# Kernel optimization log

Hardware: AMD Instinct MI355X
Metric: run time of the kernel (lower is better)

Reference implementation:

```python
import jax, jax.numpy as jnp
import numpy as np

C = 128  # n_filters; input channels must equal n_filters due to residual


def setup_inputs() -> dict:
    key = jax.random.key(0)
    kx, kw = jax.random.split(key)
    x = jax.random.normal(kx, (8, 64, 512, C), dtype=jnp.float32)
    # 1x1 conv, no bias == dense over channel axis: [C, 2C]
    W_qkv = jax.random.normal(kw, (C, 2 * C), dtype=jnp.float32) * (1.0 / np.sqrt(C))
    return {"x": x, "W_qkv": W_qkv}


def reference(x, W_qkv):
    # qkv: [B,H,W,2C]; split -> qk [B,H,W,C] -> q,k [B,H,W,C/2]; v [B,H,W,C]
    qkv = jnp.einsum('bhwc,cd->bhwd', x, W_qkv)
    half = C // 2
    q = qkv[..., :half]
    k = qkv[..., half:C]
    v = qkv[..., C:]
    # scores over the W (time) axis; NOTE: original applies no 1/sqrt(d) scaling
    scores = jnp.einsum('bhqc,bhkc->bhqk', q, k)  # [B,H,W,W]
    w = jax.nn.softmax(scores, axis=-1)
    y = jnp.einsum('bhqk,bhkc->bhqc', w, v)  # [B,H,W,C]
    y = x + y  # with_skip_connection=True
    return (y, w)
```

## Files before the change

kernel.cpp:

```cpp
#include <hip/hip_runtime.h>
#include <hip/hip_bf16.h>

typedef short s16x8 __attribute__((ext_vector_type(8)));
typedef float f32x4 __attribute__((ext_vector_type(4)));

#define MFMA_BF16(a,b,c) __builtin_amdgcn_mfma_f32_16x16x32_bf16((a),(b),(c),0,0,0)

static __device__ __forceinline__ unsigned short f2bf(float f){
  unsigned u = __builtin_bit_cast(unsigned, f);
  u += 0x7fffu + ((u >> 16) & 1u);
  return (unsigned short)(u >> 16);
}
static __device__ __forceinline__ float bf2f(unsigned short h){
  unsigned u = ((unsigned)h) << 16;
  return __builtin_bit_cast(float, u);
}
static __device__ __forceinline__ int swzi(int row, int col, int lw){
  const int chunk = (col >> 3) ^ ((row ^ (row >> 3)) & 7);
  return row*lw + (chunk << 3) + (col & 7);
}

__global__ __launch_bounds__(128) void k0_wt(const float* __restrict__ W,
                                             unsigned short* __restrict__ wtH,
                                             unsigned short* __restrict__ wtL){
  const int n = blockIdx.x;
  const int c = threadIdx.x;
  const float v = W[(size_t)c*256 + n];
  const unsigned short h = f2bf(v);
  wtH[n*128 + c] = h;
  wtL[n*128 + c] = f2bf(v - bf2f(h));
}

__global__ __launch_bounds__(512,2) void k1_qkv(const float* __restrict__ x,
    const unsigned short* __restrict__ wtH, const unsigned short* __restrict__ wtL,
    unsigned short* __restrict__ qh, unsigned short* __restrict__ ql,
    unsigned short* __restrict__ kh, unsigned short* __restrict__ kl,
    unsigned short* __restrict__ vT){
  __shared__ unsigned short xh[16384], xl[16384];
  const int t = threadIdx.x;
  const int lane = t & 63, wid = t >> 6;
  const int li = lane & 15, g = lane >> 4;
  const int m0 = blockIdx.x * 128;
  const int wm = wid >> 2, wn = wid & 3;

  {
    const int row = t >> 2, cb = (t & 3) * 32;
    const float* src = x + (size_t)(m0 + row)*128 + cb;
    #pragma unroll
    for (int gg = 0; gg < 4; ++gg){
      const float4 v0 = ((const float4*)src)[2*gg];
      const float4 v1 = ((const float4*)src)[2*gg + 1];
      const float vv[8] = {v0.x,v0.y,v0.z,v0.w,v1.x,v1.y,v1.z,v1.w};
      s16x8 h, l;
      #pragma unroll
      for (int j = 0; j < 8; ++j){
        const unsigned short hb = f2bf(vv[j]);
        h[j] = (short)hb;
        l[j] = (short)f2bf(vv[j] - bf2f(hb));
      }
      const int idx = swzi(row, cb + 8*gg, 128);
      *(s16x8*)&xh[idx] = h;
      *(s16x8*)&xl[idx] = l;
    }
  }
  __syncthreads();

  {
    f32x4 acc[4][2] = {};
    #pragma unroll
    for (int ks = 0; ks < 4; ++ks){
      const int col = ks*32 + g*8;
      s16x8 ah[4], al[4];
      #pragma unroll
      for (int mi = 0; mi < 4; ++mi){
        const int idx = swzi(wm*64 + mi*16 + li, col, 128);
        ah[mi] = *(const s16x8*)&xh[idx];
        al[mi] = *(const s16x8*)&xl[idx];
      }
      #pragma unroll
      for (int ni = 0; ni < 2; ++ni){
        const size_t boff = (size_t)(wn*32 + ni*16 + li)*128 + col;
        const s16x8 bh = *(const s16x8*)(wtH + boff);
        const s16x8 bl = *(const s16x8*)(wtL + boff);
        #pragma unroll
        for (int mi = 0; mi < 4; ++mi){
          acc[mi][ni] = MFMA_BF16(bh, ah[mi], acc[mi][ni]);
          acc[mi][ni] = MFMA_BF16(bh, al[mi], acc[mi][ni]);
          acc[mi][ni] = MFMA_BF16(bl, ah[mi], acc[mi][ni]);
        }
      }
    }
    #pragma unroll
    for (int mi = 0; mi < 4; ++mi)
      #pragma unroll
      for (int ni = 0; ni < 2; ++ni){
        const int pos = m0 + wm*64 + mi*16 + li;
        const int och = wn*32 + ni*16 + g*4;
        ushort4 hv, lv;
        #pragma unroll
        for (int r = 0; r < 4; ++r){
          const float v = acc[mi][ni][r];
          const unsigned short hb = f2bf(v);
          ((unsigned short*)&hv)[r] = hb;
          ((unsigned short*)&lv)[r] = f2bf(v - bf2f(hb));
        }
        const size_t off = (size_t)pos*64 + (och & 63);
        if (wn < 2){ *(ushort4*)&qh[off] = hv; *(ushort4*)&ql[off] = lv; }
        else       { *(ushort4*)&kh[off] = hv; *(ushort4*)&kl[off] = lv; }
      }
  }

  {
    f32x4 acc[4][2] = {};
    #pragma unroll
    for (int ks = 0; ks < 4; ++ks){
      const int col = ks*32 + g*8;
      s16x8 ah[4], al[4];
      #pragma unroll
      for (int mi = 0; mi < 4; ++mi){
        const int idx = swzi(wm*64 + mi*16 + li, col, 128);
        ah[mi] = *(const s16x8*)&xh[idx];
        al[mi] = *(const s16x8*)&xl[idx];
      }
      #pragma unroll
      for (int ni = 0; ni < 2; ++ni){
        const size_t boff = (size_t)(128 + wn*32 + ni*16 + li)*128 + col;
        const s16x8 bh = *(const s16x8*)(wtH + boff);
        const s16x8 bl = *(const s16x8*)(wtL + boff);
        #pragma unroll
        for (int mi = 0; mi < 4; ++mi){
          acc[mi][ni] = MFMA_BF16(ah[mi], bh, acc[mi][ni]);
          acc[mi][ni] = MFMA_BF16(ah[mi], bl, acc[mi][ni]);
          acc[mi][ni] = MFMA_BF16(al[mi], bh, acc[mi][ni]);
        }
      }
    }
    #pragma unroll
    for (int mi = 0; mi < 4; ++mi)
      #pragma unroll
      for (int ni = 0; ni < 2; ++ni){
        const int growb = m0 + wm*64 + mi*16 + g*4;
        const int ch = wn*32 + ni*16 + li;
        const int head = growb >> 9, posb = growb & 511;
        ushort4 pv;
        #pragma unroll
        for (int r = 0; r < 4; ++r)
          ((unsigned short*)&pv)[r] = f2bf(acc[mi][ni][r]);
        *(ushort4*)&vT[((size_t)head << 16) + ch*512 + posb] = pv;
      }
  }
}

__global__ __launch_bounds__(256,4) void k2_attn(
    const unsigned short* __restrict__ qh, const unsigned short* __restrict__ ql,
    const unsigned short* __restrict__ kh, const unsigned short* __restrict__ kl,
    const unsigned short* __restrict__ vT, const float* __restrict__ x,
    float* __restrict__ y, float* __restrict__ wout){
  __shared__ unsigned short wlds[16384];
  __shared__ float redm[128], reds[128];

  const int t = threadIdx.x;
  const int lane = t & 63, wid = t >> 6;
  const int li = lane & 15, g = lane >> 4;
  const int bi = blockIdx.x;
  const int head = (bi & 7) + 8 * (bi >> 7);
  const int qt = (bi >> 3) & 15;
  const size_t hbase = (size_t)head * 512;
  const int q0 = qt * 32;
  const int kbase = wid * 128;

  f32x4 acc[2][8] = {};
  #pragma unroll
  for (int ks = 0; ks < 2; ++ks){
    const int col = ks*32 + g*8;
    s16x8 qbh[2], qbl[2];
    #pragma unroll
    for (int qj = 0; qj < 2; ++qj){
      const size_t aoff = (hbase + q0 + qj*16 + li)*64 + col;
      qbh[qj] = *(const s16x8*)(qh + aoff);
      qbl[qj] = *(const s16x8*)(ql + aoff);
    }
    #pragma unroll
    for (int ni = 0; ni < 8; ++ni){
      const size_t boff = (hbase + kbase + ni*16 + li)*64 + col;
      const s16x8 ah = *(const s16x8*)(kh + boff);
      const s16x8 al = *(const s16x8*)(kl + boff);
      #pragma unroll
      for (int qj = 0; qj < 2; ++qj){
        acc[qj][ni] = MFMA_BF16(ah, qbh[qj], acc[qj][ni]);
        acc[qj][ni] = MFMA_BF16(al, qbh[qj], acc[qj][ni]);
        acc[qj][ni] = MFMA_BF16(ah, qbl[qj], acc[qj][ni]);
      }
    }
  }

  float fsc[2];
  #pragma unroll
  for (int qj = 0; qj < 2; ++qj){
    float m = acc[qj][0][0];
    #pragma unroll
    for (int ni = 0; ni < 8; ++ni)
      #pragma unroll
      for (int r = 0; r < 4; ++r) m = fmaxf(m, acc[qj][ni][r]);
    m = fmaxf(m, __shfl_xor(m, 16));
    m = fmaxf(m, __shfl_xor(m, 32));
    float s = 0.f;
    #pragma unroll
    for (int ni = 0; ni < 8; ++ni)
      #pragma unroll
      for (int r = 0; r < 4; ++r){
        const float e = __expf(acc[qj][ni][r] - m);
        acc[qj][ni][r] = e;
        s += e;
      }
    s += __shfl_xor(s, 16);
    s += __shfl_xor(s, 32);
    if (g == 0){
      redm[(qj*16 + li)*4 + wid] = m;
      reds[(qj*16 + li)*4 + wid] = s;
    }
    fsc[qj] = m;
  }
  __syncthreads();
  #pragma unroll
  for (int qj = 0; qj < 2; ++qj){
    const int row = qj*16 + li;
    const f32x4 mv = *(const f32x4*)&redm[row*4];
    const f32x4 sv = *(const f32x4*)&reds[row*4];
    const float M = fmaxf(fmaxf(mv[0], mv[1]), fmaxf(mv[2], mv[3]));
    const float S = sv[0]*__expf(mv[0] - M) + sv[1]*__expf(mv[1] - M)
                  + sv[2]*__expf(mv[2] - M) + sv[3]*__expf(mv[3] - M);
    fsc[qj] = __expf(fsc[qj] - M) / S;
  }

  #pragma unroll
  for (int qj = 0; qj < 2; ++qj){
    const int row = qj*16 + li;
    float* wrow = wout + (hbase + q0 + row)*512;
    #pragma unroll
    for (int ni = 0; ni < 8; ++ni){
      const int col = kbase + ni*16 + g*4;
      f32x4 wv;
      ushort4 pv;
      #pragma unroll
      for (int r = 0; r < 4; ++r){
        const float v = acc[qj][ni][r] * fsc[qj];
        wv[r] = v;
        ((unsigned short*)&pv)[r] = f2bf(v);
      }
      *(f32x4*)&wrow[col] = wv;
      *(ushort4*)&wlds[swzi(row, col, 512)] = pv;
    }
  }
  __syncthreads();

  const int c0 = wid * 32;
  f32x4 yacc[2][2] = {};
  #pragma unroll
  for (int kt = 0; kt < 16; ++kt){
    const int kp0 = kt*32 + g*8;
    s16x8 aw[2], vb[2];
    #pragma unroll
    for (int mi = 0; mi < 2; ++mi)
      aw[mi] = *(const s16x8*)&wlds[swzi(mi*16 + li, kp0, 512)];
    #pragma unroll
    for (int ci = 0; ci < 2; ++ci)
      vb[ci] = *(const s16x8*)&vT[((size_t)head << 16) + (size_t)(c0 + ci*16 + li)*512 + kp0];
    #pragma unroll
    for (int ci = 0; ci < 2; ++ci)
      #pragma unroll
      for (int mi = 0; mi < 2; ++mi)
        yacc[ci][mi] = MFMA_BF16(vb[ci], aw[mi], yacc[ci][mi]);
  }

  #pragma unroll
  for (int ci = 0; ci < 2; ++ci)
    #pragma unroll
    for (int mi = 0; mi < 2; ++mi){
      const int row = mi*16 + li;
      const size_t idx = (hbase + q0 + row)*128 + c0 + ci*16 + g*4;
      const f32x4 xv = __builtin_nontemporal_load((const f32x4*)&x[idx]);
      f32x4 ov;
      ov[0] = xv[0] + yacc[ci][mi][0];
      ov[1] = xv[1] + yacc[ci][mi][1];
      ov[2] = xv[2] + yacc[ci][mi][2];
      ov[3] = xv[3] + yacc[ci][mi][3];
      *(f32x4*)&y[idx] = ov;
    }
}

extern "C" void kernel_launch(void* const* d_in, const int* in_sizes, int n_in,
                              void* d_out, int out_size, void* d_ws, size_t ws_size,
                              hipStream_t stream){
  (void)in_sizes; (void)n_in; (void)out_size; (void)ws_size;
  const float* x = (const float*)d_in[0];
  const float* W = (const float*)d_in[1];
  float* y    = (float*)d_out;
  float* wout = y + (size_t)33554432;

  char* ws = (char*)d_ws;
  unsigned short* qh  = (unsigned short*)(ws);
  unsigned short* ql  = (unsigned short*)(ws +  33554432ull);
  unsigned short* kh  = (unsigned short*)(ws +  67108864ull);
  unsigned short* kl  = (unsigned short*)(ws + 100663296ull);
  unsigned short* vT  = (unsigned short*)(ws + 134217728ull);
  unsigned short* wtH = (unsigned short*)(ws + 201326592ull);
  unsigned short* wtL = (unsigned short*)(ws + 201392128ull);

  hipLaunchKernelGGL(k0_wt,   dim3(256),  dim3(128), 0, stream, W, wtH, wtL);
  hipLaunchKernelGGL(k1_qkv,  dim3(2048), dim3(512), 0, stream, x, wtH, wtL,
                     qh, ql, kh, kl, vT);
  hipLaunchKernelGGL(k2_attn, dim3(8192), dim3(256), 0, stream,
                     qh, ql, kh, kl, vT, x, y, wout);
}
```

Baseline: 573.4 us.

## Enlarge attention tile to 64 queries per block with 8 waves

The attention kernel now handles 64 query rows per block with 512 threads (8 waves) instead of 32 rows with 4 waves. Each wave covers 64 keys in the score phase and 16 value channels in the PV phase. The aim is to halve the number of times K and V tiles are re-read per head, at the cost of twice the LDS per block, fewer resident blocks, and an 8-way cross-wave softmax reduction.

```diff
diff --git a/kernel.cpp b/kernel.cpp
--- a/kernel.cpp
+++ b/kernel.cpp
@@ -151,42 +151,42 @@
   }
 }
 
-__global__ __launch_bounds__(256,4) void k2_attn(
+__global__ __launch_bounds__(512,2) void k2_attn(
     const unsigned short* __restrict__ qh, const unsigned short* __restrict__ ql,
     const unsigned short* __restrict__ kh, const unsigned short* __restrict__ kl,
     const unsigned short* __restrict__ vT, const float* __restrict__ x,
     float* __restrict__ y, float* __restrict__ wout){
-  __shared__ unsigned short wlds[16384];
-  __shared__ float redm[128], reds[128];
+  __shared__ unsigned short wlds[32768];
+  __shared__ float redm[512], reds[512];
 
   const int t = threadIdx.x;
   const int lane = t & 63, wid = t >> 6;
   const int li = lane & 15, g = lane >> 4;
   const int bi = blockIdx.x;
-  const int head = (bi & 7) + 8 * (bi >> 7);
-  const int qt = (bi >> 3) & 15;
+  const int head = (bi & 7) + 8 * (bi >> 6);
+  const int qt = (bi >> 3) & 7;
   const size_t hbase = (size_t)head * 512;
-  const int q0 = qt * 32;
-  const int kbase = wid * 128;
-
-  f32x4 acc[2][8] = {};
+  const int q0 = qt * 64;
+  const int kbase = wid * 64;
+
+  f32x4 acc[4][4] = {};
   #pragma unroll
   for (int ks = 0; ks < 2; ++ks){
     const int col = ks*32 + g*8;
-    s16x8 qbh[2], qbl[2];
-    #pragma unroll
-    for (int qj = 0; qj < 2; ++qj){
+    s16x8 qbh[4], qbl[4];
+    #pragma unroll
+    for (int qj = 0; qj < 4; ++qj){
       const size_t aoff = (hbase + q0 + qj*16 + li)*64 + col;
       qbh[qj] = *(const s16x8*)(qh + aoff);
       qbl[qj] = *(const s16x8*)(ql + aoff);
     }
     #pragma unroll
-    for (int ni = 0; ni < 8; ++ni){
+    for (int ni = 0; ni < 4; ++ni){
       const size_t boff = (hbase + kbase + ni*16 + li)*64 + col;
       const s16x8 ah = *(const s16x8*)(kh + boff);
       const s16x8 al = *(const s16x8*)(kl + boff);
       #pragma unroll
-      for (int qj = 0; qj < 2; ++qj){
+      for (int qj = 0; qj < 4; ++qj){
         acc[qj][ni] = MFMA_BF16(ah, qbh[qj], acc[qj][ni]);
         acc[qj][ni] = MFMA_BF16(al, qbh[qj], acc[qj][ni]);
         acc[qj][ni] = MFMA_BF16(ah, qbl[qj], acc[qj][ni]);
@@ -194,19 +194,19 @@
     }
   }
 
-  float fsc[2];
-  #pragma unroll
-  for (int qj = 0; qj < 2; ++qj){
+  float fsc[4];
+  #pragma unroll
+  for (int qj = 0; qj < 4; ++qj){
     float m = acc[qj][0][0];
     #pragma unroll
-    for (int ni = 0; ni < 8; ++ni)
+    for (int ni = 0; ni < 4; ++ni)
       #pragma unroll
       for (int r = 0; r < 4; ++r) m = fmaxf(m, acc[qj][ni][r]);
     m = fmaxf(m, __shfl_xor(m, 16));
     m = fmaxf(m, __shfl_xor(m, 32));
     float s = 0.f;
     #pragma unroll
-    for (int ni = 0; ni < 8; ++ni)
+    for (int ni = 0; ni < 4; ++ni)
       #pragma unroll
       for (int r = 0; r < 4; ++r){
         const float e = __expf(acc[qj][ni][r] - m);
@@ -216,29 +216,34 @@
     s += __shfl_xor(s, 16);
     s += __shfl_xor(s, 32);
     if (g == 0){
-      redm[(qj*16 + li)*4 + wid] = m;
-      reds[(qj*16 + li)*4 + wid] = s;
+      redm[(qj*16 + li)*8 + wid] = m;
+      reds[(qj*16 + li)*8 + wid] = s;
     }
     fsc[qj] = m;
   }
   __syncthreads();
   #pragma unroll
-  for (int qj = 0; qj < 2; ++qj){
+  for (int qj = 0; qj < 4; ++qj){
     const int row = qj*16 + li;
-    const f32x4 mv = *(const f32x4*)&redm[row*4];
-    const f32x4 sv = *(const f32x4*)&reds[row*4];
-    const float M = fmaxf(fmaxf(mv[0], mv[1]), fmaxf(mv[2], mv[3]));
-    const float S = sv[0]*__expf(mv[0] - M) + sv[1]*__expf(mv[1] - M)
-                  + sv[2]*__expf(mv[2] - M) + sv[3]*__expf(mv[3] - M);
+    const f32x4 m0v = *(const f32x4*)&redm[row*8];
+    const f32x4 m1v = *(const f32x4*)&redm[row*8 + 4];
+    const f32x4 s0v = *(const f32x4*)&reds[row*8];
+    const f32x4 s1v = *(const f32x4*)&reds[row*8 + 4];
+    float M = fmaxf(fmaxf(fmaxf(m0v[0], m0v[1]), fmaxf(m0v[2], m0v[3])),
+                    fmaxf(fmaxf(m1v[0], m1v[1]), fmaxf(m1v[2], m1v[3])));
+    float S = s0v[0]*__expf(m0v[0] - M) + s0v[1]*__expf(m0v[1] - M)
+            + s0v[2]*__expf(m0v[2] - M) + s0v[3]*__expf(m0v[3] - M)
+            + s1v[0]*__expf(m1v[0] - M) + s1v[1]*__expf(m1v[1] - M)
+            + s1v[2]*__expf(m1v[2] - M) + s1v[3]*__expf(m1v[3] - M);
     fsc[qj] = __expf(fsc[qj] - M) / S;
   }
 
   #pragma unroll
-  for (int qj = 0; qj < 2; ++qj){
+  for (int qj = 0; qj < 4; ++qj){
     const int row = qj*16 + li;
     float* wrow = wout + (hbase + q0 + row)*512;
     #pragma unroll
-    for (int ni = 0; ni < 8; ++ni){
+    for (int ni = 0; ni < 4; ++ni){
       const int col = kbase + ni*16 + g*4;
       f32x4 wv;
       ushort4 pv;
@@ -254,39 +259,32 @@
   }
   __syncthreads();
 
-  const int c0 = wid * 32;
-  f32x4 yacc[2][2] = {};
+  const int c0 = wid * 16;
+  f32x4 yacc[4] = {};
+  const unsigned short* vhead = vT + ((size_t)head << 16) + (size_t)(c0 + li)*512;
   #pragma unroll
   for (int kt = 0; kt < 16; ++kt){
     const int kp0 = kt*32 + g*8;
-    s16x8 aw[2], vb[2];
-    #pragma unroll
-    for (int mi = 0; mi < 2; ++mi)
-      aw[mi] = *(const s16x8*)&wlds[swzi(mi*16 + li, kp0, 512)];
-    #pragma unroll
-    for (int ci = 0; ci < 2; ++ci)
-      vb[ci] = *(const s16x8*)&vT[((size_t)head << 16) + (size_t)(c0 + ci*16 + li)*512 + kp0];
-    #pragma unroll
-    for (int ci = 0; ci < 2; ++ci)
-      #pragma unroll
-      for (int mi = 0; mi < 2; ++mi)
-        yacc[ci][mi] = MFMA_BF16(vb[ci], aw[mi], yacc[ci][mi]);
-  }
-
-  #pragma unroll
-  for (int ci = 0; ci < 2; ++ci)
-    #pragma unroll
-    for (int mi = 0; mi < 2; ++mi){
-      const int row = mi*16 + li;
-      const size_t idx = (hbase + q0 + row)*128 + c0 + ci*16 + g*4;
-      const f32x4 xv = __builtin_nontemporal_load((const f32x4*)&x[idx]);
-      f32x4 ov;
-      ov[0] = xv[0] + yacc[ci][mi][0];
-      ov[1] = xv[1] + yacc[ci][mi][1];
-      ov[2] = xv[2] + yacc[ci][mi][2];
-      ov[3] = xv[3] + yacc[ci][mi][3];
-      *(f32x4*)&y[idx] = ov;
-    }
+    const s16x8 vb = *(const s16x8*)&vhead[kp0];
+    #pragma unroll
+    for (int mi = 0; mi < 4; ++mi){
+      const s16x8 aw = *(const s16x8*)&wlds[swzi(mi*16 + li, kp0, 512)];
+      yacc[mi] = MFMA_BF16(vb, aw, yacc[mi]);
+    }
+  }
+
+  #pragma unroll
+  for (int mi = 0; mi < 4; ++mi){
+    const int row = mi*16 + li;
+    const size_t idx = (hbase + q0 + row)*128 + c0 + g*4;
+    const f32x4 xv = __builtin_nontemporal_load((const f32x4*)&x[idx]);
+    f32x4 ov;
+    ov[0] = xv[0] + yacc[mi][0];
+    ov[1] = xv[1] + yacc[mi][1];
+    ov[2] = xv[2] + yacc[mi][2];
+    ov[3] = xv[3] + yacc[mi][3];
+    *(f32x4*)&y[idx] = ov;
+  }
 }
 
 extern "C" void kernel_launch(void* const* d_in, const int* in_sizes, int n_in,
@@ -310,6 +308,6 @@
   hipLaunchKernelGGL(k0_wt,   dim3(256),  dim3(128), 0, stream, W, wtH, wtL);
   hipLaunchKernelGGL(k1_qkv,  dim3(2048), dim3(512), 0, stream, x, wtH, wtL,
                      qh, ql, kh, kl, vT);
-  hipLaunchKernelGGL(k2_attn, dim3(8192), dim3(256), 0, stream,
+  hipLaunchKernelGGL(k2_attn, dim3(4096), dim3(512), 0, stream,
                      qh, ql, kh, kl, vT, x, y, wout);
 }
```

Result: faster. 518.4 us (-9.6%).
